# Optimization experiments

Hardware: AMD Instinct MI355X
Metric: run time of the kernel (lower is better)

The kernel has to match this reference:

```python
import jax, jax.numpy as jnp
import numpy as np

DECAY = 0.9


def setup_inputs() -> dict:
    key = jax.random.key(0)
    ks = jax.random.split(key, 8)
    B, L, d_model = 4, 2048, 1024
    d_state = 16
    d_inner = 2 * d_model  # expand=2
    x = jax.random.normal(ks[0], (B, L, d_model), dtype=jnp.float32)
    Win = jax.random.normal(ks[1], (d_model, d_inner), dtype=jnp.float32) / np.sqrt(d_model)
    bin_ = jnp.zeros((d_inner,), dtype=jnp.float32)
    Bp = jax.random.normal(ks[2], (d_inner, d_state), dtype=jnp.float32) * 0.01
    Cp = jax.random.normal(ks[3], (d_state, d_inner), dtype=jnp.float32) * 0.01
    Dp = jnp.ones((d_inner,), dtype=jnp.float32)
    Wout = jax.random.normal(ks[4], (d_inner, d_model), dtype=jnp.float32) / np.sqrt(d_inner)
    bout = jnp.zeros((d_model,), dtype=jnp.float32)
    return {"x": x, "Win": Win, "bin_": bin_, "Bp": Bp, "Cp": Cp, "Dp": Dp,
            "Wout": Wout, "bout": bout}


def reference(x, Win, bin_, Bp, Cp, Dp, Wout, bout):
    # x: [B, L, d_model]
    B, L, _ = x.shape
    d_inner, d_state = Bp.shape
    xi = jax.nn.silu(x @ Win + bin_)          # [B, L, d_inner]
    xt_seq = jnp.swapaxes(xi, 0, 1)            # [L, B, d_inner] for scan over time

    def step(h, xt):
        # h: [B, d_inner, d_state]; xt: [B, d_inner]
        h = h * DECAY + xt[:, :, None] * Bp[None, :, :]
        y = jnp.einsum('bij,ji->bi', h, Cp) + Dp * xt
        return h, y

    h0 = jnp.zeros((B, d_inner, d_state), dtype=x.dtype)
    _, ys = jax.lax.scan(step, h0, xt_seq)     # ys: [L, B, d_inner]
    y = jnp.swapaxes(ys, 0, 1)                 # [B, L, d_inner]
    return y @ Wout + bout                     # [B, L, d_model]
```

## Files before the change

### kernel.cpp

```cpp
#include <hip/hip_runtime.h>
#include <hip/hip_bf16.h>
#include <cstdint>
#include <cstddef>

typedef __attribute__((ext_vector_type(8))) short short8_t;
typedef __attribute__((ext_vector_type(4))) float f32x4;

__device__ __forceinline__ void gload16(const void* g, void* l) {
  __builtin_amdgcn_global_load_lds(
      (const __attribute__((address_space(1))) void*)g,
      (__attribute__((address_space(3))) void*)l, 16, 0, 0);
}

#define BARRIER() do { asm volatile("" ::: "memory"); __builtin_amdgcn_s_barrier(); asm volatile("" ::: "memory"); } while (0)
#define WVM4 asm volatile("s_waitcnt vmcnt(4)" ::: "memory")
#define WVM3 asm volatile("s_waitcnt vmcnt(3)" ::: "memory")
#define WVM0 asm volatile("s_waitcnt vmcnt(0)" ::: "memory")

__global__ __launch_bounds__(256) void cvt_bf16_kernel(
    const float* __restrict__ in, __hip_bfloat16* __restrict__ out, int n) {
  int gid = blockIdx.x * blockDim.x + threadIdx.x;
  int idx = gid * 4;
  if (idx >= n) return;
  float4 v = *reinterpret_cast<const float4*>(in + idx);
  union { short4 s4; __hip_bfloat16 h[4]; } u;
  u.h[0] = __float2bfloat16(v.x);
  u.h[1] = __float2bfloat16(v.y);
  u.h[2] = __float2bfloat16(v.z);
  u.h[3] = __float2bfloat16(v.w);
  *reinterpret_cast<short4*>(out + idx) = u.s4;
}

__global__ __launch_bounds__(256) void transpose_cvt_kernel(
    const float* __restrict__ in, __hip_bfloat16* __restrict__ out, int R, int C) {
  __shared__ float tile[32][33];
  int c0 = blockIdx.x * 32, r0 = blockIdx.y * 32;
  int tx = threadIdx.x, ty = threadIdx.y;
#pragma unroll
  for (int j = 0; j < 32; j += 8)
    tile[ty + j][tx] = in[(size_t)(r0 + ty + j) * C + c0 + tx];
  __syncthreads();
#pragma unroll
  for (int j = 0; j < 32; j += 8)
    out[(size_t)(c0 + ty + j) * R + r0 + tx] = __float2bfloat16(tile[tx][ty + j]);
}

template <int NF, int EPI>
__global__ __launch_bounds__(512, 2) void gemm8p_kernel(
    const __hip_bfloat16* __restrict__ A,
    const __hip_bfloat16* __restrict__ Bt,
    const float* __restrict__ bias,
    void* __restrict__ Cout,
    int M, int N, int K) {
  constexpr int BN = NF * 64;
  constexpr int NB = NF / 2;
  constexpr int BUNIT = BN * 64;
  constexpr int ABYTES = 65536;
  constexpr int LDSB = ABYTES + 4 * BUNIT;
  __shared__ int4 ldsv[LDSB / 16];
  char* lds = (char*)ldsv;

  const int tid = threadIdx.x;
  const int l = tid & 63;
  const int w = tid >> 6;
  const int wm = w >> 2, wn = w & 3;
  const int fr = l & 15;
  const int sl = ((l >> 4) ^ ((fr >> 3) << 1)) * 16;
  const int arow_base = (wm * 128 + fr) * 64 + sl;
  const int brow_base = (wn * (16 * NF) + fr) * 64 + sl;

  const int nbn = N / BN;
  int bid = blockIdx.x;
  const int cpx = gridDim.x >> 3;
  bid = (bid & 7) * cpx + (bid >> 3);
  const int brow = (bid / nbn) * 256;
  const int bcol = (bid % nbn) * BN;

  int adst[2], ar[2], acb[2];
#pragma unroll
  for (int j = 0; j < 2; ++j) {
    int d = j * 8192 + w * 1024 + l * 16;
    int lg = d ^ (((d >> 9) & 1) << 5);
    adst[j] = j * 8192 + w * 1024;
    ar[j] = lg >> 6;
    acb[j] = lg & 63;
  }

  const char* Abp = (const char*)A;
  const char* Bbp = (const char*)Bt;

  auto stA = [&](int buf, int kh, int tt) {
#pragma unroll
    for (int j = 0; j < 2; ++j) {
      const char* src = Abp + ((size_t)(brow + ar[j]) * K + tt * 64 + kh * 32) * 2 + acb[j];
      gload16(src, lds + buf * 32768 + kh * 16384 + adst[j]);
    }
  };
  auto stB = [&](int buf, int kh, int tt) {
#pragma unroll
    for (int j = 0; j < NB; ++j) {
      const char* src = Bbp + ((size_t)(bcol + ar[j]) * K + tt * 64 + kh * 32) * 2 + acb[j];
      gload16(src, lds + ABYTES + buf * 2 * BUNIT + kh * BUNIT + adst[j]);
    }
  };

  f32x4 acc[8][NF];
#pragma unroll
  for (int m = 0; m < 8; ++m)
#pragma unroll
    for (int n = 0; n < NF; ++n) acc[m][n] = (f32x4)0.f;
  short8_t af[4], bf[NF];

  auto ldA_ = [&](int buf, int kh, int mh) {
#pragma unroll
    for (int mi = 0; mi < 4; ++mi)
      af[mi] = *(const short8_t*)(lds + buf * 32768 + kh * 16384 + arow_base + (mh * 4 + mi) * 1024);
  };
  auto ldB_ = [&](int buf, int kh) {
#pragma unroll
    for (int n = 0; n < NF; ++n)
      bf[n] = *(const short8_t*)(lds + ABYTES + buf * 2 * BUNIT + kh * BUNIT + brow_base + n * 1024);
  };
  auto mfma_ = [&](int mh) {
    __builtin_amdgcn_s_setprio(1);
#pragma unroll
    for (int mi = 0; mi < 4; ++mi)
#pragma unroll
      for (int n = 0; n < NF; ++n)
        acc[mh * 4 + mi][n] =
            __builtin_amdgcn_mfma_f32_16x16x32_bf16(af[mi], bf[n], acc[mh * 4 + mi][n], 0, 0, 0);
    __builtin_amdgcn_s_setprio(0);
  };

  const int NT = K >> 6;
  stA(0, 0, 0); stB(0, 0, 0); stA(0, 1, 0); stB(0, 1, 0);
  stA(1, 0, 1); stB(1, 0, 1);
  if constexpr (NB == 2) { WVM4; } else { WVM3; }
  BARRIER();

  for (int it = 0; it < NT / 2 - 1; ++it) {
    const int T = 2 * it;
    ldA_(0,0,0); ldB_(0,0); stA(1,1,T+1); BARRIER(); mfma_(0); BARRIER();
    ldA_(0,0,1);            stB(1,1,T+1); BARRIER(); mfma_(1); BARRIER();
    ldA_(0,1,0); ldB_(0,1); stA(0,0,T+2); BARRIER(); mfma_(0); BARRIER();
    ldA_(0,1,1);            stB(0,0,T+2); BARRIER(); mfma_(1);
    if constexpr (NB == 2) { WVM4; } else { WVM3; }
    BARRIER();
    ldA_(1,0,0); ldB_(1,0); stA(0,1,T+2); BARRIER(); mfma_(0); BARRIER();
    ldA_(1,0,1);            stB(0,1,T+2); BARRIER(); mfma_(1); BARRIER();
    ldA_(1,1,0); ldB_(1,1); stA(1,0,T+3); BARRIER(); mfma_(0); BARRIER();
    ldA_(1,1,1);            stB(1,0,T+3); BARRIER(); mfma_(1);
    if constexpr (NB == 2) { WVM4; } else { WVM3; }
    BARRIER();
  }
  {
    const int T = NT - 2;
    ldA_(0,0,0); ldB_(0,0); stA(1,1,T+1); BARRIER(); mfma_(0); BARRIER();
    ldA_(0,0,1);            stB(1,1,T+1); BARRIER(); mfma_(1); BARRIER();
    ldA_(0,1,0); ldB_(0,1); BARRIER(); mfma_(0); BARRIER();
    ldA_(0,1,1);            BARRIER(); mfma_(1); WVM0; BARRIER();
    ldA_(1,0,0); ldB_(1,0); BARRIER(); mfma_(0); BARRIER();
    ldA_(1,0,1);            BARRIER(); mfma_(1); BARRIER();
    ldA_(1,1,0); ldB_(1,1); BARRIER(); mfma_(0); BARRIER();
    ldA_(1,1,1);            BARRIER(); mfma_(1);
  }

  const int r0 = brow + wm * 128 + (l >> 4) * 4;
  const int c0 = bcol + wn * (16 * NF) + fr;
#pragma unroll
  for (int m = 0; m < 8; ++m) {
#pragma unroll
    for (int n = 0; n < NF; ++n) {
      const int col = c0 + n * 16;
      const float bv = bias[col];
#pragma unroll
      for (int j = 0; j < 4; ++j) {
        const int row = r0 + m * 16 + j;
        float v = acc[m][n][j] + bv;
        if constexpr (EPI == 0) {
          v = v / (1.0f + __expf(-v));
          ((__hip_bfloat16*)Cout)[(size_t)row * N + col] = __float2bfloat16(v);
        } else {
          ((float*)Cout)[(size_t)row * N + col] = v;
        }
      }
    }
  }
}

__global__ __launch_bounds__(256) void scan_kernel(
    const __hip_bfloat16* __restrict__ xi,
    const float* __restrict__ Bp,
    const float* __restrict__ Cp,
    const float* __restrict__ Dp,
    __hip_bfloat16* __restrict__ y) {
  constexpr int L = 2048, DI = 2048, DS = 16, TW = 256, H = 96;
  const int tid = threadIdx.x;
  const int bidx = blockIdx.x;
  const int iblk = bidx & 7;
  const int chunk = (bidx >> 3) & 7;
  const int b = bidx >> 6;
  const int i = iblk * 256 + tid;

  float cb = 0.f;
#pragma unroll
  for (int s = 0; s < DS; ++s) cb += Bp[i * DS + s] * Cp[s * DI + i];
  const float dp = Dp[i];

  const int t0 = chunk * TW;
  int tstart = t0 - H;
  if (tstart < 0) tstart = 0;

  const __hip_bfloat16* xp = xi + (size_t)(b * L) * DI + i;
  __hip_bfloat16* yp = y + (size_t)(b * L) * DI + i;

  float g = 0.f;
  const __hip_bfloat16* p = xp + (size_t)tstart * DI;
  for (int t = tstart; t < t0; ++t, p += DI)
    g = g * 0.9f + __bfloat162float(*p);
  __hip_bfloat16* q = yp + (size_t)t0 * DI;
  for (int t = 0; t < TW; ++t, p += DI, q += DI) {
    float xv = __bfloat162float(*p);
    g = g * 0.9f + xv;
    *q = __float2bfloat16(cb * g + dp * xv);
  }
}

extern "C" void kernel_launch(void* const* d_in, const int* in_sizes, int n_in,
                              void* d_out, int out_size, void* d_ws, size_t ws_size,
                              hipStream_t stream) {
  const float* x    = (const float*)d_in[0];
  const float* Win  = (const float*)d_in[1];
  const float* bin  = (const float*)d_in[2];
  const float* Bp   = (const float*)d_in[3];
  const float* Cp   = (const float*)d_in[4];
  const float* Dp   = (const float*)d_in[5];
  const float* Wout = (const float*)d_in[6];
  const float* bout = (const float*)d_in[7];
  float* out = (float*)d_out;

  constexpr int Bb = 4, L = 2048, DM = 1024, DI = 2048;
  constexpr int Mrows = Bb * L;

  char* ws = (char*)d_ws;
  __hip_bfloat16* xb    = (__hip_bfloat16*)ws;
  __hip_bfloat16* WinT  = (__hip_bfloat16*)(ws + (16u << 20));
  __hip_bfloat16* WoutT = (__hip_bfloat16*)(ws + (20u << 20));
  __hip_bfloat16* xi    = (__hip_bfloat16*)(ws + (24u << 20));
  __hip_bfloat16* yb    = (__hip_bfloat16*)(ws + (56u << 20));

  {
    int n = Mrows * DM;
    cvt_bf16_kernel<<<n / 1024, 256, 0, stream>>>(x, xb, n);
  }
  transpose_cvt_kernel<<<dim3(DI / 32, DM / 32), dim3(32, 8), 0, stream>>>(Win, WinT, DM, DI);
  transpose_cvt_kernel<<<dim3(DM / 32, DI / 32), dim3(32, 8), 0, stream>>>(Wout, WoutT, DI, DM);
  gemm8p_kernel<4, 0><<<(Mrows / 256) * (DI / 256), 512, 0, stream>>>(
      xb, WinT, bin, (void*)xi, Mrows, DI, DM);
  scan_kernel<<<Bb * (L / 256) * (DI / 256), 256, 0, stream>>>(xi, Bp, Cp, Dp, yb);
  gemm8p_kernel<2, 1><<<(Mrows / 256) * (DM / 128), 512, 0, stream>>>(
      yb, WoutT, bout, (void*)out, Mrows, DM, DI);
}
```

Before: 137.6 us.

## Restructure GEMM pipeline into two phases per k-half and shorten scan warmup

The GEMM main loop goes from eight barrier-separated phases per two k-tiles (half the A fragments per MFMA burst) to two phases per k-tile. Each phase loads all eight A fragments and the B fragments, issues the next k-half's global-to-LDS loads, then runs one larger MFMA block. This halves barrier count per k-tile and lengthens MFMA bursts, at the cost of more live fragment registers and shorter prefetch distance. Separately, the scan kernel's chunk warmup history H drops from 96 to 32 steps, cutting redundant recurrence work and relying on 0.9^32 decay being small enough for accuracy.

```diff
diff --git a/kernel.cpp b/kernel.cpp
--- a/kernel.cpp
+++ b/kernel.cpp
@@ -13,9 +13,8 @@
 }
 
 #define BARRIER() do { asm volatile("" ::: "memory"); __builtin_amdgcn_s_barrier(); asm volatile("" ::: "memory"); } while (0)
-#define WVM4 asm volatile("s_waitcnt vmcnt(4)" ::: "memory")
-#define WVM3 asm volatile("s_waitcnt vmcnt(3)" ::: "memory")
-#define WVM0 asm volatile("s_waitcnt vmcnt(0)" ::: "memory")
+#define LGKM0 asm volatile("s_waitcnt lgkmcnt(0)" ::: "memory")
+#define WVM(n) asm volatile("s_waitcnt vmcnt(" #n ")" ::: "memory")
 
 __global__ __launch_bounds__(256) void cvt_bf16_kernel(
     const float* __restrict__ in, __hip_bfloat16* __restrict__ out, int n) {
@@ -46,7 +45,7 @@
 }
 
 template <int NF, int EPI>
-__global__ __launch_bounds__(512, 2) void gemm8p_kernel(
+__global__ __launch_bounds__(512, 2) void gemm2p_kernel(
     const __hip_bfloat16* __restrict__ A,
     const __hip_bfloat16* __restrict__ Bt,
     const float* __restrict__ bias,
@@ -54,10 +53,9 @@
     int M, int N, int K) {
   constexpr int BN = NF * 64;
   constexpr int NB = NF / 2;
-  constexpr int BUNIT = BN * 64;
-  constexpr int ABYTES = 65536;
-  constexpr int LDSB = ABYTES + 4 * BUNIT;
-  __shared__ int4 ldsv[LDSB / 16];
+  constexpr int AUNIT = 16384, BUNIT = NF * 4096;
+  constexpr int BOFF = 4 * AUNIT;
+  __shared__ int4 ldsv[(4 * AUNIT + 4 * BUNIT) / 16];
   char* lds = (char*)ldsv;
 
   const int tid = threadIdx.x;
@@ -66,8 +64,8 @@
   const int wm = w >> 2, wn = w & 3;
   const int fr = l & 15;
   const int sl = ((l >> 4) ^ ((fr >> 3) << 1)) * 16;
-  const int arow_base = (wm * 128 + fr) * 64 + sl;
-  const int brow_base = (wn * (16 * NF) + fr) * 64 + sl;
+  const int arowb = (wm * 128 + fr) * 64 + sl;
+  const int browb = (wn * (16 * NF) + fr) * 64 + sl;
 
   const int nbn = N / BN;
   int bid = blockIdx.x;
@@ -75,33 +73,33 @@
   bid = (bid & 7) * cpx + (bid >> 3);
   const int brow = (bid / nbn) * 256;
   const int bcol = (bid % nbn) * BN;
-
-  int adst[2], ar[2], acb[2];
+  const size_t K2 = (size_t)K * 2;
+
+  int arA[2], acbA[2], dstA[2];
 #pragma unroll
   for (int j = 0; j < 2; ++j) {
     int d = j * 8192 + w * 1024 + l * 16;
     int lg = d ^ (((d >> 9) & 1) << 5);
-    adst[j] = j * 8192 + w * 1024;
-    ar[j] = lg >> 6;
-    acb[j] = lg & 63;
+    arA[j] = lg >> 6;  acbA[j] = lg & 63;
+    dstA[j] = j * 8192 + w * 1024;
   }
 
   const char* Abp = (const char*)A;
   const char* Bbp = (const char*)Bt;
 
-  auto stA = [&](int buf, int kh, int tt) {
-#pragma unroll
-    for (int j = 0; j < 2; ++j) {
-      const char* src = Abp + ((size_t)(brow + ar[j]) * K + tt * 64 + kh * 32) * 2 + acb[j];
-      gload16(src, lds + buf * 32768 + kh * 16384 + adst[j]);
-    }
-  };
-  auto stB = [&](int buf, int kh, int tt) {
-#pragma unroll
-    for (int j = 0; j < NB; ++j) {
-      const char* src = Bbp + ((size_t)(bcol + ar[j]) * K + tt * 64 + kh * 32) * 2 + acb[j];
-      gload16(src, lds + ABYTES + buf * 2 * BUNIT + kh * BUNIT + adst[j]);
-    }
+  auto stA = [&](int t, int kh) {
+    const int base = (t & 1) * 2 * AUNIT + kh * AUNIT;
+#pragma unroll
+    for (int j = 0; j < 2; ++j)
+      gload16(Abp + (size_t)(brow + arA[j]) * K2 + t * 128 + kh * 64 + acbA[j],
+              lds + base + dstA[j]);
+  };
+  auto stB = [&](int t, int kh) {
+    const int base = BOFF + (t & 1) * 2 * BUNIT + kh * BUNIT;
+#pragma unroll
+    for (int j = 0; j < NB; ++j)
+      gload16(Bbp + (size_t)(bcol + arA[j]) * K2 + t * 128 + kh * 64 + acbA[j],
+              lds + base + dstA[j]);
   };
 
   f32x4 acc[8][NF];
@@ -109,60 +107,68 @@
   for (int m = 0; m < 8; ++m)
 #pragma unroll
     for (int n = 0; n < NF; ++n) acc[m][n] = (f32x4)0.f;
-  short8_t af[4], bf[NF];
-
-  auto ldA_ = [&](int buf, int kh, int mh) {
-#pragma unroll
-    for (int mi = 0; mi < 4; ++mi)
-      af[mi] = *(const short8_t*)(lds + buf * 32768 + kh * 16384 + arow_base + (mh * 4 + mi) * 1024);
-  };
-  auto ldB_ = [&](int buf, int kh) {
+  short8_t af[8], bf[NF];
+
+  auto ldAB = [&](int buf, int kh) {
+    const int ab = buf * 2 * AUNIT + kh * AUNIT;
+#pragma unroll
+    for (int mi = 0; mi < 8; ++mi)
+      af[mi] = *(const short8_t*)(lds + ab + arowb + mi * 1024);
+    const int bb = BOFF + buf * 2 * BUNIT + kh * BUNIT;
 #pragma unroll
     for (int n = 0; n < NF; ++n)
-      bf[n] = *(const short8_t*)(lds + ABYTES + buf * 2 * BUNIT + kh * BUNIT + brow_base + n * 1024);
-  };
-  auto mfma_ = [&](int mh) {
+      bf[n] = *(const short8_t*)(lds + bb + browb + n * 1024);
+  };
+  auto mfmaC = [&]() {
     __builtin_amdgcn_s_setprio(1);
 #pragma unroll
-    for (int mi = 0; mi < 4; ++mi)
+    for (int mi = 0; mi < 8; ++mi)
 #pragma unroll
       for (int n = 0; n < NF; ++n)
-        acc[mh * 4 + mi][n] =
-            __builtin_amdgcn_mfma_f32_16x16x32_bf16(af[mi], bf[n], acc[mh * 4 + mi][n], 0, 0, 0);
+        acc[mi][n] = __builtin_amdgcn_mfma_f32_16x16x32_bf16(af[mi], bf[n], acc[mi][n], 0, 0, 0);
     __builtin_amdgcn_s_setprio(0);
   };
+  auto wvm_steady = [&]() { if constexpr (NF == 4) { WVM(8); } else { WVM(6); } };
+  auto wvm_half   = [&]() { if constexpr (NF == 4) { WVM(4); } else { WVM(3); } };
 
   const int NT = K >> 6;
-  stA(0, 0, 0); stB(0, 0, 0); stA(0, 1, 0); stB(0, 1, 0);
-  stA(1, 0, 1); stB(1, 0, 1);
-  if constexpr (NB == 2) { WVM4; } else { WVM3; }
-  BARRIER();
-
-  for (int it = 0; it < NT / 2 - 1; ++it) {
-    const int T = 2 * it;
-    ldA_(0,0,0); ldB_(0,0); stA(1,1,T+1); BARRIER(); mfma_(0); BARRIER();
-    ldA_(0,0,1);            stB(1,1,T+1); BARRIER(); mfma_(1); BARRIER();
-    ldA_(0,1,0); ldB_(0,1); stA(0,0,T+2); BARRIER(); mfma_(0); BARRIER();
-    ldA_(0,1,1);            stB(0,0,T+2); BARRIER(); mfma_(1);
-    if constexpr (NB == 2) { WVM4; } else { WVM3; }
-    BARRIER();
-    ldA_(1,0,0); ldB_(1,0); stA(0,1,T+2); BARRIER(); mfma_(0); BARRIER();
-    ldA_(1,0,1);            stB(0,1,T+2); BARRIER(); mfma_(1); BARRIER();
-    ldA_(1,1,0); ldB_(1,1); stA(1,0,T+3); BARRIER(); mfma_(0); BARRIER();
-    ldA_(1,1,1);            stB(1,0,T+3); BARRIER(); mfma_(1);
-    if constexpr (NB == 2) { WVM4; } else { WVM3; }
-    BARRIER();
+  stA(0, 0); stB(0, 0); stA(0, 1); stB(0, 1); stA(1, 0); stB(1, 0);
+  wvm_half(); BARRIER();
+
+  for (int t = 0; t < NT - 2; ++t) {
+    const int buf = t & 1;
+    ldAB(buf, 0);
+    stA(t + 1, 1); stB(t + 1, 1);
+    BARRIER(); LGKM0;
+    mfmaC();
+    wvm_steady(); BARRIER();
+    ldAB(buf, 1);
+    stA(t + 2, 0); stB(t + 2, 0);
+    BARRIER(); LGKM0;
+    mfmaC();
+    wvm_steady(); BARRIER();
   }
   {
-    const int T = NT - 2;
-    ldA_(0,0,0); ldB_(0,0); stA(1,1,T+1); BARRIER(); mfma_(0); BARRIER();
-    ldA_(0,0,1);            stB(1,1,T+1); BARRIER(); mfma_(1); BARRIER();
-    ldA_(0,1,0); ldB_(0,1); BARRIER(); mfma_(0); BARRIER();
-    ldA_(0,1,1);            BARRIER(); mfma_(1); WVM0; BARRIER();
-    ldA_(1,0,0); ldB_(1,0); BARRIER(); mfma_(0); BARRIER();
-    ldA_(1,0,1);            BARRIER(); mfma_(1); BARRIER();
-    ldA_(1,1,0); ldB_(1,1); BARRIER(); mfma_(0); BARRIER();
-    ldA_(1,1,1);            BARRIER(); mfma_(1);
+    const int buf = (NT - 2) & 1;
+    ldAB(buf, 0);
+    stA(NT - 1, 1); stB(NT - 1, 1);
+    BARRIER(); LGKM0;
+    mfmaC();
+    wvm_steady(); BARRIER();
+    ldAB(buf, 1);
+    BARRIER(); LGKM0;
+    mfmaC();
+    wvm_half(); BARRIER();
+  }
+  {
+    const int buf = (NT - 1) & 1;
+    ldAB(buf, 0);
+    BARRIER(); LGKM0;
+    mfmaC();
+    WVM(0); BARRIER();
+    ldAB(buf, 1);
+    BARRIER(); LGKM0;
+    mfmaC();
   }
 
   const int r0 = brow + wm * 128 + (l >> 4) * 4;
@@ -194,7 +200,7 @@
     const float* __restrict__ Cp,
     const float* __restrict__ Dp,
     __hip_bfloat16* __restrict__ y) {
-  constexpr int L = 2048, DI = 2048, DS = 16, TW = 256, H = 96;
+  constexpr int L = 2048, DI = 2048, DS = 16, TW = 256, H = 32;
   const int tid = threadIdx.x;
   const int bidx = blockIdx.x;
   const int iblk = bidx & 7;
@@ -255,9 +261,9 @@
   }
   transpose_cvt_kernel<<<dim3(DI / 32, DM / 32), dim3(32, 8), 0, stream>>>(Win, WinT, DM, DI);
   transpose_cvt_kernel<<<dim3(DM / 32, DI / 32), dim3(32, 8), 0, stream>>>(Wout, WoutT, DI, DM);
-  gemm8p_kernel<4, 0><<<(Mrows / 256) * (DI / 256), 512, 0, stream>>>(
+  gemm2p_kernel<4, 0><<<(Mrows / 256) * (DI / 256), 512, 0, stream>>>(
       xb, WinT, bin, (void*)xi, Mrows, DI, DM);
   scan_kernel<<<Bb * (L / 256) * (DI / 256), 256, 0, stream>>>(xi, Bp, Cp, Dp, yb);
-  gemm8p_kernel<2, 1><<<(Mrows / 256) * (DM / 128), 512, 0, stream>>>(
+  gemm2p_kernel<2, 1><<<(Mrows / 256) * (DM / 128), 512, 0, stream>>>(
       yb, WoutT, bout, (void*)out, Mrows, DM, DI);
 }
```

Measured after the change: 124.8 us. 9.3% less time.
